# Performance work log

Hardware: AMD Instinct MI355X
Metric: run time of the kernel (lower is better)

Reference implementation:

```python
import jax, jax.numpy as jnp
import numpy as np

ALPHA = 0.2  # LeakyReLU slope
EPS = 1e-16


def _spgat_layer(x, W, a, row, col, N, concat):
    # h: [N, d]
    h = x @ W
    d = h.shape[1]
    # edge attention: a^T [h_row || h_col]  (pyGAT SpGAT: exp(-leakyrelu(.)))
    f_src = h @ a[:d]   # [N]
    f_dst = h @ a[d:]   # [N]
    e = jnp.exp(-jax.nn.leaky_relu(f_src[row] + f_dst[col], ALPHA))  # [E]
    denom = jax.ops.segment_sum(e, row, num_segments=N) + EPS        # [N]
    num = jax.ops.segment_sum(e[:, None] * h[col], row, num_segments=N)  # [N, d]
    out = num / denom[:, None]
    return jax.nn.elu(out) if concat else out


def _spgat(x, W1, a1, W2, a2, edges):
    row, col = edges[0], edges[1]
    N = x.shape[0]
    h = _spgat_layer(x, W1, a1, row, col, N, concat=True)
    h = _spgat_layer(h, W2, a2, row, col, N, concat=False)
    return jax.nn.elu(h)


def setup_inputs() -> dict:
    key = jax.random.key(0)
    ks = jax.random.split(key, 20)
    VOCAB, NFEAT = 50000, 300
    N_TW, L = 50000, 16
    UV = 50000
    E = 800000
    HID, JOINT, NCLASS = 64, 128, 2
    B = 4096

    inp = {}
    # integer structure (constants)
    inp['features_index'] = jax.random.randint(ks[0], (N_TW, L), 0, VOCAB, dtype=jnp.int32)
    inp['tw_edges'] = jax.random.randint(ks[1], (2, E), 0, N_TW, dtype=jnp.int32)
    inp['ut_edges'] = jax.random.randint(ks[2], (2, E), 0, UV, dtype=jnp.int32)
    inp['tw_graph_idx'] = jax.random.randint(ks[3], (B,), 0, N_TW, dtype=jnp.int32)
    inp['ut_graph_idx'] = jax.random.randint(ks[4], (B,), 0, UV, dtype=jnp.int32)
    # learned parameters
    inp['word_emb'] = jax.random.normal(ks[5], (VOCAB, NFEAT), jnp.float32) * 0.1
    inp['user_emb'] = jax.random.normal(ks[6], (UV, NFEAT), jnp.float32) * 0.1
    def gat_params(k, din, dh, dout):
        k1, k2, k3, k4 = jax.random.split(k, 4)
        return (jax.random.normal(k1, (din, dh), jnp.float32) * (1.0 / np.sqrt(din)),
                jax.random.normal(k2, (2 * dh,), jnp.float32) * 0.1,
                jax.random.normal(k3, (dh, dout), jnp.float32) * (1.0 / np.sqrt(dh)),
                jax.random.normal(k4, (2 * dout,), jnp.float32) * 0.1)
    inp['tw_W1'], inp['tw_a1'], inp['tw_W2'], inp['tw_a2'] = gat_params(ks[7], NFEAT, HID, JOINT)
    inp['tu_W1'], inp['tu_a1'], inp['tu_W2'], inp['tu_a2'] = gat_params(ks[8], NFEAT, HID, JOINT)
    inp['weight_W'] = jax.random.uniform(ks[9], (JOINT, JOINT), jnp.float32, -0.1, 0.1)
    inp['weight_proj'] = jax.random.uniform(ks[10], (JOINT, 1), jnp.float32, -0.1, 0.1)
    inp['out_W'] = jax.random.normal(ks[11], (NCLASS, JOINT), jnp.float32) * (1.0 / np.sqrt(JOINT))
    inp['out_b'] = jnp.zeros((NCLASS,), jnp.float32)
    return inp


def reference(word_emb, user_emb, tw_W1, tw_a1, tw_W2, tw_a2,
              tu_W1, tu_a1, tu_W2, tu_a2, weight_W, weight_proj,
              out_W, out_b, features_index, tw_edges, ut_edges,
              tw_graph_idx, ut_graph_idx):
    # tweet features: mean of word embeddings per tweet  [N_tw, nfeat]
    twt_X = word_emb[features_index].mean(axis=1)
    tw_X = _spgat(twt_X, tw_W1, tw_a1, tw_W2, tw_a2, tw_edges)   # [N_tw, joint]
    tu_X = _spgat(user_emb, tu_W1, tu_a1, tu_W2, tu_a2, ut_edges)  # [uV, joint]
    # attention-weighted fusion of the two views
    u_tw = jnp.tanh(tw_X @ weight_W)
    u_tu = jnp.tanh(tu_X @ weight_W)
    att_tw = jnp.mean(u_tw @ weight_proj, axis=0)  # [1]
    att_tu = jnp.mean(u_tu @ weight_proj, axis=0)  # [1]
    att = jax.nn.softmax(jnp.concatenate([att_tw, att_tu], axis=0))  # [2]
    feat = att[0] * tw_X[tw_graph_idx] + att[1] * tu_X[ut_graph_idx]  # [B, joint]
    logits = feat @ out_W.T + out_b
    return jax.nn.log_softmax(logits, axis=1)
```

## Files before the change

### kernel.cpp

```cpp
#include <hip/hip_runtime.h>
#include <hip/hip_bf16.h>

typedef __hip_bfloat16 bf16;
typedef unsigned int uint32;
typedef __attribute__((ext_vector_type(8))) short s8v;
typedef __attribute__((ext_vector_type(4))) short s4v;
typedef __attribute__((ext_vector_type(8))) short bf8v;
typedef __attribute__((ext_vector_type(4))) float f4v;

#define CAP 64
#define CAPSH 6

__device__ __forceinline__ float waveReduce(float v) {
#pragma unroll
    for (int o = 32; o > 0; o >>= 1) v += __shfl_xor(v, o, 64);
    return v;
}

__device__ __forceinline__ short f2bf(float x) {
    __hip_bfloat16 h = __float2bfloat16(x);
    return *reinterpret_cast<short*>(&h);
}
__device__ __forceinline__ float bf2f(short s) {
    return __uint_as_float(((uint32)(unsigned short)s) << 16);
}
__device__ __forceinline__ uint32 pack2(float x, float y) {
    return (uint32)(unsigned short)f2bf(x) | (((uint32)(unsigned short)f2bf(y)) << 16);
}
__device__ __forceinline__ float blo(uint32 d) { return __uint_as_float(d << 16); }
__device__ __forceinline__ float bhi(uint32 d) { return __uint_as_float(d & 0xffff0000u); }
__device__ __forceinline__ float felu(float x) { return x > 0.f ? x : __expf(x) - 1.f; }

struct WJobs {
    const float* src[5];
    short* dst[5];
    int K[5], N[5], KP[5], total[5];
    int* cursor;
    float* attsum;
    int N2;
};
__global__ void wtrans_all(WJobs jb) {
    int j = blockIdx.y;
    int i = blockIdx.x * blockDim.x + threadIdx.x;
    if (j == 5) {
        if (i < jb.N2) jb.cursor[i] = i << CAPSH;
        if (i < 2) jb.attsum[i] = 0.f;
        return;
    }
    if (i >= jb.total[j]) return;
    int KP = jb.KP[j];
    int n = i / KP, k = i - n * KP;
    jb.dst[j][i] = f2bf(k < jb.K[j] ? jb.src[j][(size_t)k * jb.N[j] + n] : 0.f);
}

struct GJob {
    const void* A;
    const short* Wt;
    const float* av;
    void* C;
    float* fs;
    float* fd;
    int M;
};
struct SJob {
    const int* rowA; const int* colA;
    const int* rowB; const int* colB;
    int* cursor; int* ecol;
    int E; int NTW; int nbg;
};

template <typename AT, int K, int KPAD, int N, int CSTORE, bool DO_F, bool DO_ATT, bool DO_SCAT>
__global__ __launch_bounds__(256) void mfma_gemm(GJob j0, GJob j1, int nb0,
                                                 float* __restrict__ attsum, int bnd, SJob sj) {
    constexpr int NT = N / 16;
    constexpr int NP = KPAD / 64;
    int t = threadIdx.x;

    if constexpr (DO_SCAT) {
        if ((int)blockIdx.x >= sj.nbg) {
            int i = ((int)blockIdx.x - sj.nbg) * 256 + t;
            if (i < sj.E) {
                int r = sj.rowA[i];
                int p0 = atomicAdd(&sj.cursor[r], 1);
                if (p0 < (r << CAPSH) + CAP) sj.ecol[p0] = sj.colA[i];
            } else if (i < 2 * sj.E) {
                int r = sj.NTW + sj.rowB[i - sj.E];
                int p0 = atomicAdd(&sj.cursor[r], 1);
                if (p0 < (r << CAPSH) + CAP) sj.ecol[p0] = sj.colB[i - sj.E];
            }
            return;
        }
    }

    __shared__ short As[64 * 72];
    __shared__ short Ws[N * 72];
    __shared__ float red[8];
    int lane = t & 63;
    int wid = t >> 6;
    int col = lane & 15;
    int quad = lane >> 4;

    int bid = blockIdx.x;
    bool sec = bid >= nb0;
    GJob J = sec ? j1 : j0;
    const AT* A = (const AT*)J.A;
    const short* Wt = J.Wt;
    const float* av = J.av;
    int M = J.M;
    int row0 = (sec ? bid - nb0 : bid) * 64;

    f4v acc[NT];
#pragma unroll
    for (int i = 0; i < NT; ++i) { f4v z = {0.f, 0.f, 0.f, 0.f}; acc[i] = z; }

    float4 ra[4];
    s8v rsa[2];
    s8v rb[NT / 2];

    auto issue = [&](int p) {
        int k0 = p * 64;
        if constexpr (sizeof(AT) == 4) {
            const float4* A4 = (const float4*)A;
            int f = t & 15, r0 = t >> 4;
#pragma unroll
            for (int r = 0; r < 4; ++r) {
                int gr = row0 + r0 + 16 * r;
                int f4i = (k0 >> 2) + f;
                float4 v = {0.f, 0.f, 0.f, 0.f};
                if (gr < M && f4i < K / 4) v = A4[(size_t)gr * (K / 4) + f4i];
                ra[r] = v;
            }
        } else {
            int c8 = t & 7, r0 = t >> 3;
#pragma unroll
            for (int r = 0; r < 2; ++r) {
                int gr = row0 + r0 + 32 * r;
                s8v v = {0, 0, 0, 0, 0, 0, 0, 0};
                if (gr < M) v = *(const s8v*)&A[(size_t)gr * K + k0 + c8 * 8];
                rsa[r] = v;
            }
        }
        {
            int c8 = t & 7, r0 = t >> 3;
#pragma unroll
            for (int r = 0; r < NT / 2; ++r)
                rb[r] = *(const s8v*)&Wt[(size_t)(r0 + 32 * r) * KPAD + k0 + c8 * 8];
        }
    };
    auto commit = [&]() {
        if constexpr (sizeof(AT) == 4) {
            int f = t & 15, r0 = t >> 4;
#pragma unroll
            for (int r = 0; r < 4; ++r) {
                float4 v = ra[r];
                s4v sv = {f2bf(v.x), f2bf(v.y), f2bf(v.z), f2bf(v.w)};
                *(s4v*)&As[(r0 + 16 * r) * 72 + f * 4] = sv;
            }
        } else {
            int c8 = t & 7, r0 = t >> 3;
#pragma unroll
            for (int r = 0; r < 2; ++r) *(s8v*)&As[(r0 + 32 * r) * 72 + c8 * 8] = rsa[r];
        }
        int c8 = t & 7, r0 = t >> 3;
#pragma unroll
        for (int r = 0; r < NT / 2; ++r) *(s8v*)&Ws[(r0 + 32 * r) * 72 + c8 * 8] = rb[r];
    };

    issue(0);
    for (int p = 0; p < NP; ++p) {
        __syncthreads();
        commit();
        __syncthreads();
        if (p + 1 < NP) issue(p + 1);
#pragma unroll
        for (int c2 = 0; c2 < 2; ++c2) {
            int ko = c2 * 32 + quad * 8;
            bf8v af = *(const bf8v*)&As[(wid * 16 + col) * 72 + ko];
#pragma unroll
            for (int nt = 0; nt < NT; ++nt) {
                bf8v bf = *(const bf8v*)&Ws[(nt * 16 + col) * 72 + ko];
                acc[nt] = __builtin_amdgcn_mfma_f32_16x16x32_bf16(af, bf, acc[nt], 0, 0, 0);
            }
        }
    }

    int mbase = row0 + wid * 16;
    if constexpr (CSTORE == 1) {
        float* C = (float*)J.C;
#pragma unroll
        for (int nt = 0; nt < NT; ++nt)
#pragma unroll
            for (int r = 0; r < 4; ++r) {
                int gr = mbase + quad * 4 + r;
                if (gr < M) C[(size_t)gr * N + nt * 16 + col] = acc[nt][r];
            }
    } else if constexpr (CSTORE == 2) {
        short* C = (short*)J.C;
#pragma unroll
        for (int nt = 0; nt < NT; ++nt)
#pragma unroll
            for (int r = 0; r < 4; ++r) {
                int gr = mbase + quad * 4 + r;
                if (gr < M) C[(size_t)gr * N + nt * 16 + col] = f2bf(acc[nt][r]);
            }
    }
    if constexpr (DO_F) {
        if (av) {
            float* fs = J.fs;
            float* fd = J.fd;
            float a0[NT], a1[NT];
#pragma unroll
            for (int nt = 0; nt < NT; ++nt) {
                a0[nt] = av[nt * 16 + col];
                a1[nt] = av[N + nt * 16 + col];
            }
#pragma unroll
            for (int r = 0; r < 4; ++r) {
                float p0 = 0.f, p1 = 0.f;
#pragma unroll
                for (int nt = 0; nt < NT; ++nt) {
                    p0 += acc[nt][r] * a0[nt];
                    p1 += acc[nt][r] * a1[nt];
                }
#pragma unroll
                for (int o = 8; o > 0; o >>= 1) {
                    p0 += __shfl_xor(p0, o, 64);
                    p1 += __shfl_xor(p1, o, 64);
                }
                int gr = mbase + quad * 4 + r;
                if (col == 0 && gr < M) { fs[gr] = p0; fd[gr] = p1; }
            }
        }
    }
    if constexpr (DO_ATT) {
        float s0 = 0.f, s1 = 0.f;
#pragma unroll
        for (int nt = 0; nt < NT; ++nt) {
            float pj = av[nt * 16 + col];
#pragma unroll
            for (int r = 0; r < 4; ++r) {
                int gr = mbase + quad * 4 + r;
                float v = tanhf(acc[nt][r]) * pj;
                if (gr < bnd) s0 += v; else s1 += v;
            }
        }
        s0 = waveReduce(s0);
        s1 = waveReduce(s1);
        if (lane == 0) { red[wid] = s0; red[4 + wid] = s1; }
        __syncthreads();
        if (t == 0) {
            atomicAdd(attsum + 0, red[0] + red[1] + red[2] + red[3]);
            atomicAdd(attsum + 1, red[4] + red[5] + red[6] + red[7]);
        }
    }
}

__global__ void gather_h64(const int* __restrict__ idx, const uint32* __restrict__ P,
                           const float* __restrict__ a,
                           short* __restrict__ H, float* __restrict__ fsv, float* __restrict__ fdv,
                           int N) {
    int wv = (blockIdx.x * blockDim.x + threadIdx.x) >> 6;
    int lane = threadIdx.x & 63;
    if (wv >= N) return;
    int hf = lane >> 5, li = lane & 31;
    const int* ip = idx + wv * 16;
    float a0 = 0.f, a1 = 0.f;
#pragma unroll
    for (int t = 0; t < 8; ++t) {
        int ind = ip[2 * t + hf];
        uint32 d = P[(size_t)ind * 32 + li];
        a0 += blo(d);
        a1 += bhi(d);
    }
    a0 += __shfl_xor(a0, 32, 64);
    a1 += __shfl_xor(a1, 32, 64);
    a0 *= 0.0625f;
    a1 *= 0.0625f;
    if (hf == 0) ((uint32*)H)[(size_t)wv * 32 + li] = pack2(a0, a1);
    float cp = hf ? 0.f : (a0 * a[2 * li] + a1 * a[2 * li + 1]);
    float cq = hf ? 0.f : (a0 * a[64 + 2 * li] + a1 * a[64 + 2 * li + 1]);
    float p = waveReduce(cp);
    float q = waveReduce(cq);
    if (lane == 0) { fsv[wv] = p; fdv[wv] = q; }
}

__global__ void agg64f_kernel(const int* __restrict__ cursor, const int* __restrict__ ecol,
                              const float* __restrict__ fs, const float* __restrict__ fd,
                              const uint32* __restrict__ hb, uint32* __restrict__ out,
                              int N2, int NTW) {
    int wv = (blockIdx.x * blockDim.x + threadIdx.x) >> 6;
    int lane = threadIdx.x & 63;
    if (wv >= N2) return;
    int s = wv << CAPSH;
    int ne = min(cursor[wv] - s, CAP);
    int coff = wv < NTW ? 0 : NTW;
    float fsr = fs[wv];
    int cl = 0;
    float el = 0.f;
    if (lane < ne) {
        cl = ecol[s + lane];
        float f = fsr + fd[coff + cl];
        el = __expf(-(f >= 0.f ? f : 0.2f * f));
    }
    int qd = lane >> 4, li = lane & 15;
    const uint2* h2 = (const uint2*)hb;
    float a0 = 0.f, a1 = 0.f, a2 = 0.f, a3 = 0.f, den = 0.f;
    for (int kb = 0; kb < ne; kb += 16) {
        int k0 = kb + qd, k1 = kb + 4 + qd, k2 = kb + 8 + qd, k3 = kb + 12 + qd;
        int c0 = __shfl(cl, k0, 64); float e0 = __shfl(el, k0, 64);
        int c1 = __shfl(cl, k1, 64); float e1 = __shfl(el, k1, 64);
        int c2 = __shfl(cl, k2, 64); float e2 = __shfl(el, k2, 64);
        int c3 = __shfl(cl, k3, 64); float e3 = __shfl(el, k3, 64);
        uint2 d0 = h2[(size_t)(coff + c0) * 16 + li];
        uint2 d1 = h2[(size_t)(coff + c1) * 16 + li];
        uint2 d2 = h2[(size_t)(coff + c2) * 16 + li];
        uint2 d3 = h2[(size_t)(coff + c3) * 16 + li];
        a0 += e0 * blo(d0.x) + e1 * blo(d1.x) + e2 * blo(d2.x) + e3 * blo(d3.x);
        a1 += e0 * bhi(d0.x) + e1 * bhi(d1.x) + e2 * bhi(d2.x) + e3 * bhi(d3.x);
        a2 += e0 * blo(d0.y) + e1 * blo(d1.y) + e2 * blo(d2.y) + e3 * blo(d3.y);
        a3 += e0 * bhi(d0.y) + e1 * bhi(d1.y) + e2 * bhi(d2.y) + e3 * bhi(d3.y);
        den += e0 + e1 + e2 + e3;
    }
    a0 += __shfl_xor(a0, 16, 64); a0 += __shfl_xor(a0, 32, 64);
    a1 += __shfl_xor(a1, 16, 64); a1 += __shfl_xor(a1, 32, 64);
    a2 += __shfl_xor(a2, 16, 64); a2 += __shfl_xor(a2, 32, 64);
    a3 += __shfl_xor(a3, 16, 64); a3 += __shfl_xor(a3, 32, 64);
    den += __shfl_xor(den, 16, 64); den += __shfl_xor(den, 32, 64);
    if (lane < 16) {
        float inv = 1.f / (den + 1e-16f);
        float v0 = felu(a0 * inv);
        float v1 = felu(a1 * inv);
        float v2 = felu(a2 * inv);
        float v3 = felu(a3 * inv);
        uint2 o = {pack2(v0, v1), pack2(v2, v3)};
        ((uint2*)out)[(size_t)wv * 16 + li] = o;
    }
}

__global__ void agg128f_kernel(const int* __restrict__ cursor, const int* __restrict__ ecol,
                               const float* __restrict__ fs, const float* __restrict__ fd,
                               const uint32* __restrict__ hb, uint32* __restrict__ out,
                               int N2, int NTW) {
    int wv = (blockIdx.x * blockDim.x + threadIdx.x) >> 6;
    int lane = threadIdx.x & 63;
    if (wv >= N2) return;
    int s = wv << CAPSH;
    int ne = min(cursor[wv] - s, CAP);
    int coff = wv < NTW ? 0 : NTW;
    float fsr = fs[wv];
    int cl = 0;
    float el = 0.f;
    if (lane < ne) {
        cl = ecol[s + lane];
        float f = fsr + fd[coff + cl];
        el = __expf(-(f >= 0.f ? f : 0.2f * f));
    }
    int hf = lane >> 5, li = lane & 31;
    const uint2* h2 = (const uint2*)hb;
    float a0 = 0.f, a1 = 0.f, a2 = 0.f, a3 = 0.f, den = 0.f;
    for (int kb = 0; kb < ne; kb += 8) {
        int k0 = kb + hf, k1 = kb + 2 + hf, k2 = kb + 4 + hf, k3 = kb + 6 + hf;
        int c0 = __shfl(cl, k0, 64); float e0 = __shfl(el, k0, 64);
        int c1 = __shfl(cl, k1, 64); float e1 = __shfl(el, k1, 64);
        int c2 = __shfl(cl, k2, 64); float e2 = __shfl(el, k2, 64);
        int c3 = __shfl(cl, k3, 64); float e3 = __shfl(el, k3, 64);
        uint2 d0 = h2[(size_t)(coff + c0) * 32 + li];
        uint2 d1 = h2[(size_t)(coff + c1) * 32 + li];
        uint2 d2 = h2[(size_t)(coff + c2) * 32 + li];
        uint2 d3 = h2[(size_t)(coff + c3) * 32 + li];
        a0 += e0 * blo(d0.x) + e1 * blo(d1.x) + e2 * blo(d2.x) + e3 * blo(d3.x);
        a1 += e0 * bhi(d0.x) + e1 * bhi(d1.x) + e2 * bhi(d2.x) + e3 * bhi(d3.x);
        a2 += e0 * blo(d0.y) + e1 * blo(d1.y) + e2 * blo(d2.y) + e3 * blo(d3.y);
        a3 += e0 * bhi(d0.y) + e1 * bhi(d1.y) + e2 * bhi(d2.y) + e3 * bhi(d3.y);
        den += e0 + e1 + e2 + e3;
    }
    a0 += __shfl_xor(a0, 32, 64);
    a1 += __shfl_xor(a1, 32, 64);
    a2 += __shfl_xor(a2, 32, 64);
    a3 += __shfl_xor(a3, 32, 64);
    den += __shfl_xor(den, 32, 64);
    if (hf == 0) {
        float inv = 1.f / (den + 1e-16f);
        float v0 = felu(a0 * inv);
        float v1 = felu(a1 * inv);
        float v2 = felu(a2 * inv);
        float v3 = felu(a3 * inv);
        uint2 o = {pack2(v0, v1), pack2(v2, v3)};
        ((uint2*)out)[(size_t)wv * 32 + li] = o;
    }
}

__global__ void final_kernel(const short* __restrict__ twX, const short* __restrict__ tuX,
                             const int* __restrict__ twi, const int* __restrict__ tui,
                             const float* __restrict__ attsum,
                             const float* __restrict__ outW, const float* __restrict__ outb,
                             float* __restrict__ out, int B, float invNtw, float invNuv) {
    int wave = (blockIdx.x * blockDim.x + threadIdx.x) >> 6;
    int lane = threadIdx.x & 63;
    if (wave >= B) return;
    float z0 = attsum[0] * invNtw, z1 = attsum[1] * invNuv;
    float m = fmaxf(z0, z1);
    float e0 = expf(z0 - m), e1 = expf(z1 - m);
    float a0 = e0 / (e0 + e1), a1 = e1 / (e0 + e1);
    int ti = twi[wave], ui = tui[wave];
    float l0 = 0.f, l1 = 0.f;
#pragma unroll
    for (int p = 0; p < 2; ++p) {
        int j = lane + 64 * p;
        float feat = a0 * bf2f(twX[(size_t)ti * 128 + j]) + a1 * bf2f(tuX[(size_t)ui * 128 + j]);
        l0 += feat * outW[j];
        l1 += feat * outW[128 + j];
    }
    l0 = waveReduce(l0);
    l1 = waveReduce(l1);
    if (lane == 0) {
        l0 += outb[0];
        l1 += outb[1];
        float mm = fmaxf(l0, l1);
        float lse = mm + logf(expf(l0 - mm) + expf(l1 - mm));
        out[wave * 2 + 0] = l0 - lse;
        out[wave * 2 + 1] = l1 - lse;
    }
}

extern "C" void kernel_launch(void* const* d_in, const int* in_sizes, int n_in,
                              void* d_out, int out_size, void* d_ws, size_t ws_size,
                              hipStream_t stream) {
    const int* features_index = (const int*)d_in[0];
    const int* tw_edges = (const int*)d_in[1];
    const int* ut_edges = (const int*)d_in[2];
    const int* tw_gidx = (const int*)d_in[3];
    const int* ut_gidx = (const int*)d_in[4];
    const float* word_emb = (const float*)d_in[5];
    const float* user_emb = (const float*)d_in[6];
    const float* tw_W1 = (const float*)d_in[7];
    const float* tw_a1 = (const float*)d_in[8];
    const float* tw_W2 = (const float*)d_in[9];
    const float* tw_a2 = (const float*)d_in[10];
    const float* tu_W1 = (const float*)d_in[11];
    const float* tu_a1 = (const float*)d_in[12];
    const float* tu_W2 = (const float*)d_in[13];
    const float* tu_a2 = (const float*)d_in[14];
    const float* weight_W = (const float*)d_in[15];
    const float* weight_proj = (const float*)d_in[16];
    const float* out_W = (const float*)d_in[17];
    const float* out_b = (const float*)d_in[18];

    const int E = in_sizes[1] / 2;
    const int NTW = in_sizes[0] / 16;
    const int VOCAB = in_sizes[5] / 300;
    const int UV = in_sizes[6] / 300;
    const int B = in_sizes[3];
    const int N2 = NTW + UV;

    char* ws = (char*)d_ws;
    size_t off = 0;
    auto carve = [&](size_t bytes) -> void* {
        void* p = ws + off;
        off += (bytes + 255) & ~(size_t)255;
        return p;
    };
    float* Pbuf = (float*)carve((size_t)VOCAB * 64 * sizeof(float));
    short* Hb1 = (short*)carve((size_t)N2 * 64 * sizeof(short));
    short* H2 = (short*)carve((size_t)N2 * 128 * sizeof(short));
    short* X = (short*)carve((size_t)N2 * 128 * sizeof(short));
    float* f_s = (float*)carve((size_t)N2 * sizeof(float));
    float* f_d = (float*)carve((size_t)N2 * sizeof(float));
    float* attsum = (float*)carve(256);
    int* cursor = (int*)carve((size_t)N2 * sizeof(int));
    int* ecol = (int*)carve((size_t)N2 * CAP * sizeof(int));
    short* Wt1tw = (short*)carve((size_t)64 * 320 * sizeof(short));
    short* Wt1tu = (short*)carve((size_t)64 * 320 * sizeof(short));
    short* Wt2tw = (short*)carve((size_t)128 * 64 * sizeof(short));
    short* Wt2tu = (short*)carve((size_t)128 * 64 * sizeof(short));
    short* Wta   = (short*)carve((size_t)128 * 128 * sizeof(short));
    short* num1 = ((size_t)VOCAB * 64 * sizeof(float) >= (size_t)N2 * 64 * sizeof(short))
                      ? (short*)Pbuf
                      : (short*)carve((size_t)N2 * 64 * sizeof(short));
    (void)ws_size; (void)n_in; (void)out_size;

    WJobs jb;
    jb.src[0] = tw_W1;    jb.dst[0] = Wt1tw; jb.K[0] = 300; jb.N[0] = 64;  jb.KP[0] = 320; jb.total[0] = 64 * 320;
    jb.src[1] = tu_W1;    jb.dst[1] = Wt1tu; jb.K[1] = 300; jb.N[1] = 64;  jb.KP[1] = 320; jb.total[1] = 64 * 320;
    jb.src[2] = tw_W2;    jb.dst[2] = Wt2tw; jb.K[2] = 64;  jb.N[2] = 128; jb.KP[2] = 64;  jb.total[2] = 128 * 64;
    jb.src[3] = tu_W2;    jb.dst[3] = Wt2tu; jb.K[3] = 64;  jb.N[3] = 128; jb.KP[3] = 64;  jb.total[3] = 128 * 64;
    jb.src[4] = weight_W; jb.dst[4] = Wta;   jb.K[4] = 128; jb.N[4] = 128; jb.KP[4] = 128; jb.total[4] = 128 * 128;
    jb.cursor = cursor;
    jb.attsum = attsum;
    jb.N2 = N2;
    {
        int gx = (64 * 320 + 255) / 256;
        int gc = (N2 + 255) / 256;
        if (gc > gx) gx = gc;
        dim3 g(gx, 6);
        wtrans_all<<<g, 256, 0, stream>>>(jb);
    }

    SJob sempty{nullptr, nullptr, nullptr, nullptr, nullptr, nullptr, 0, 0, 0};

    {
        GJob a{word_emb, Wt1tw, nullptr, Pbuf, nullptr, nullptr, VOCAB};
        GJob b{user_emb, Wt1tu, tu_a1, Hb1 + (size_t)NTW * 64, f_s + NTW, f_d + NTW, UV};
        int nbw = (VOCAB + 63) / 64, nbu = (UV + 63) / 64;
        int nbg = nbw + nbu;
        int nsc = (2 * E + 255) / 256;
        SJob sj{tw_edges, tw_edges + E, ut_edges, ut_edges + E, cursor, ecol, E, NTW, nbg};
        mfma_gemm<float, 300, 320, 64, 2, true, false, true><<<nbg + nsc, 256, 0, stream>>>(
            a, b, nbw, nullptr, 0, sj);
    }
    gather_h64<<<(NTW + 3) / 4, 256, 0, stream>>>(features_index, (const uint32*)Pbuf, tw_a1,
                                                  Hb1, f_s, f_d, NTW);

    agg64f_kernel<<<(N2 + 3) / 4, 256, 0, stream>>>(cursor, ecol, f_s, f_d,
                                                    (const uint32*)Hb1, (uint32*)num1, N2, NTW);

    {
        int nbtw = (NTW + 63) / 64, nbtu = (UV + 63) / 64;
        GJob a{num1, Wt2tw, tw_a2, H2, f_s, f_d, NTW};
        GJob b{num1 + (size_t)NTW * 64, Wt2tu, tu_a2, H2 + (size_t)NTW * 128,
               f_s + NTW, f_d + NTW, UV};
        mfma_gemm<short, 64, 64, 128, 2, true, false, false><<<nbtw + nbtu, 256, 0, stream>>>(
            a, b, nbtw, nullptr, 0, sempty);
    }

    agg128f_kernel<<<(N2 + 3) / 4, 256, 0, stream>>>(cursor, ecol, f_s, f_d,
                                                     (const uint32*)H2, (uint32*)X, N2, NTW);

    {
        GJob a{X, Wta, weight_proj, nullptr, nullptr, nullptr, N2};
        int nb = (N2 + 63) / 64;
        mfma_gemm<short, 128, 128, 128, 0, false, true, false><<<nb, 256, 0, stream>>>(
            a, a, nb, attsum, NTW, sempty);
    }

    final_kernel<<<(B + 3) / 4, 256, 0, stream>>>(X, X + (size_t)NTW * 128, tw_gidx, ut_gidx,
                                                  attsum, out_W, out_b, (float*)d_out, B,
                                                  1.0f / (float)NTW, 1.0f / (float)UV);
}
```

Baseline: 486.3 us.

## Two-pass edge bucketing: stage edges by row window before CSR scatter

The direct scatter of edges into per-row slots with random global atomics is replaced by two passes. First, the GEMM-side scatter blocks bucket packed (row, col) edges into 128 staging bins keyed by row window and block slot, using wave-aggregated atomics. Then extra blocks in the gather kernel replay each bin and do the per-row cursor atomics within a localized row range, aiming for better cache locality. This adds an extra pass over the edges and a staging buffer that aliases X. It also relies on column ids fitting in 16 bits and bins not overflowing SCAP, otherwise edges are silently dropped.

```diff
diff --git a/kernel.cpp b/kernel.cpp
--- a/kernel.cpp
+++ b/kernel.cpp
@@ -10,6 +10,7 @@
 
 #define CAP 64
 #define CAPSH 6
+#define WSH 14
 
 __device__ __forceinline__ float waveReduce(float v) {
 #pragma unroll
@@ -37,6 +38,7 @@
     int K[5], N[5], KP[5], total[5];
     int* cursor;
     float* attsum;
+    int* gcount;
     int N2;
 };
 __global__ void wtrans_all(WJobs jb) {
@@ -45,6 +47,7 @@
     if (j == 5) {
         if (i < jb.N2) jb.cursor[i] = i << CAPSH;
         if (i < 2) jb.attsum[i] = 0.f;
+        if (i < 128) jb.gcount[i] = 0;
         return;
     }
     if (i >= jb.total[j]) return;
@@ -65,8 +68,8 @@
 struct SJob {
     const int* rowA; const int* colA;
     const int* rowB; const int* colB;
-    int* cursor; int* ecol;
-    int E; int NTW; int nbg;
+    uint32* stage; int* gcount;
+    int E; int NTW; int nbg; int SCAP;
 };
 
 template <typename AT, int K, int KPAD, int N, int CSTORE, bool DO_F, bool DO_ATT, bool DO_SCAT>
@@ -78,15 +81,33 @@
 
     if constexpr (DO_SCAT) {
         if ((int)blockIdx.x >= sj.nbg) {
-            int i = ((int)blockIdx.x - sj.nbg) * 256 + t;
+            int bb = (int)blockIdx.x - sj.nbg;
+            int i = bb * 256 + t;
+            int lane = t & 63;
+            int slot = bb & 15;
+            int r = -1, c = 0;
             if (i < sj.E) {
-                int r = sj.rowA[i];
-                int p0 = atomicAdd(&sj.cursor[r], 1);
-                if (p0 < (r << CAPSH) + CAP) sj.ecol[p0] = sj.colA[i];
+                r = sj.rowA[i]; c = sj.colA[i];
             } else if (i < 2 * sj.E) {
-                int r = sj.NTW + sj.rowB[i - sj.E];
-                int p0 = atomicAdd(&sj.cursor[r], 1);
-                if (p0 < (r << CAPSH) + CAP) sj.ecol[p0] = sj.colB[i - sj.E];
+                r = sj.NTW + sj.rowB[i - sj.E]; c = sj.colB[i - sj.E];
+            }
+            int w = r >> WSH;
+            uint32 val = ((uint32)(r & ((1 << WSH) - 1)) << 16) | (uint32)c;
+#pragma unroll
+            for (int k = 0; k < 8; ++k) {
+                unsigned long long m = __ballot(r >= 0 && w == k);
+                if (m == 0ull) continue;
+                int cnt = __popcll(m);
+                int lead = __ffsll((long long)m) - 1;
+                int base = 0;
+                if (lane == lead) base = atomicAdd(&sj.gcount[k * 16 + slot], cnt);
+                base = __shfl(base, lead, 64);
+                if (r >= 0 && w == k) {
+                    int myoff = __popcll(m & ((1ull << lane) - 1ull));
+                    int pos = base + myoff;
+                    if (pos < sj.SCAP)
+                        sj.stage[((size_t)(k * 16 + slot)) * sj.SCAP + pos] = val;
+                }
             }
             return;
         }
@@ -258,16 +279,37 @@
 __global__ void gather_h64(const int* __restrict__ idx, const uint32* __restrict__ P,
                            const float* __restrict__ a,
                            short* __restrict__ H, float* __restrict__ fsv, float* __restrict__ fdv,
-                           int N) {
-    int wv = (blockIdx.x * blockDim.x + threadIdx.x) >> 6;
-    int lane = threadIdx.x & 63;
+                           int N,
+                           const uint32* __restrict__ stage, const int* __restrict__ gcount,
+                           int SCAP, int* __restrict__ cursor, int* __restrict__ ecol, int nPB) {
+    int t = threadIdx.x;
+    if ((int)blockIdx.x < nPB) {
+        int b = blockIdx.x;
+        int w = b & 7;
+        int rest = b >> 3;
+        int slot = rest & 15;
+        int chunk = rest >> 4;
+        int cnt = min(gcount[w * 16 + slot], SCAP);
+        int jend = min(chunk * 4096 + 4096, cnt);
+        const uint32* sp = stage + ((size_t)(w * 16 + slot)) * SCAP;
+        for (int j = chunk * 4096 + t; j < jend; j += 256) {
+            uint32 v = sp[j];
+            int r = (w << WSH) + (int)(v >> 16);
+            int c = (int)(v & 0xffffu);
+            int p = atomicAdd(&cursor[r], 1);
+            if (p < (r << CAPSH) + CAP) ecol[p] = c;
+        }
+        return;
+    }
+    int wv = (((int)blockIdx.x - nPB) * 256 + t) >> 6;
+    int lane = t & 63;
     if (wv >= N) return;
     int hf = lane >> 5, li = lane & 31;
     const int* ip = idx + wv * 16;
     float a0 = 0.f, a1 = 0.f;
 #pragma unroll
-    for (int t = 0; t < 8; ++t) {
-        int ind = ip[2 * t + hf];
+    for (int u = 0; u < 8; ++u) {
+        int ind = ip[2 * u + hf];
         uint32 d = P[(size_t)ind * 32 + li];
         a0 += blo(d);
         a1 += bhi(d);
@@ -469,6 +511,7 @@
     float* attsum = (float*)carve(256);
     int* cursor = (int*)carve((size_t)N2 * sizeof(int));
     int* ecol = (int*)carve((size_t)N2 * CAP * sizeof(int));
+    int* gcount = (int*)carve(128 * sizeof(int));
     short* Wt1tw = (short*)carve((size_t)64 * 320 * sizeof(short));
     short* Wt1tu = (short*)carve((size_t)64 * 320 * sizeof(short));
     short* Wt2tw = (short*)carve((size_t)128 * 64 * sizeof(short));
@@ -477,6 +520,11 @@
     short* num1 = ((size_t)VOCAB * 64 * sizeof(float) >= (size_t)N2 * 64 * sizeof(short))
                       ? (short*)Pbuf
                       : (short*)carve((size_t)N2 * 64 * sizeof(short));
+    int perSlot = (2 * E) / 128;
+    int SCAP = ((perSlot * 13 / 8) + 4095) / 4096 * 4096;
+    int chunks = SCAP / 4096;
+    int nPB = 128 * chunks;
+    uint32* stage = (uint32*)X;
     (void)ws_size; (void)n_in; (void)out_size;
 
     WJobs jb;
@@ -487,6 +535,7 @@
     jb.src[4] = weight_W; jb.dst[4] = Wta;   jb.K[4] = 128; jb.N[4] = 128; jb.KP[4] = 128; jb.total[4] = 128 * 128;
     jb.cursor = cursor;
     jb.attsum = attsum;
+    jb.gcount = gcount;
     jb.N2 = N2;
     {
         int gx = (64 * 320 + 255) / 256;
@@ -496,7 +545,7 @@
         wtrans_all<<<g, 256, 0, stream>>>(jb);
     }
 
-    SJob sempty{nullptr, nullptr, nullptr, nullptr, nullptr, nullptr, 0, 0, 0};
+    SJob sempty{nullptr, nullptr, nullptr, nullptr, nullptr, nullptr, 0, 0, 0, 0};
 
     {
         GJob a{word_emb, Wt1tw, nullptr, Pbuf, nullptr, nullptr, VOCAB};
@@ -504,12 +553,14 @@
         int nbw = (VOCAB + 63) / 64, nbu = (UV + 63) / 64;
         int nbg = nbw + nbu;
         int nsc = (2 * E + 255) / 256;
-        SJob sj{tw_edges, tw_edges + E, ut_edges, ut_edges + E, cursor, ecol, E, NTW, nbg};
+        SJob sj{tw_edges, tw_edges + E, ut_edges, ut_edges + E, stage, gcount, E, NTW, nbg, SCAP};
         mfma_gemm<float, 300, 320, 64, 2, true, false, true><<<nbg + nsc, 256, 0, stream>>>(
             a, b, nbw, nullptr, 0, sj);
     }
-    gather_h64<<<(NTW + 3) / 4, 256, 0, stream>>>(features_index, (const uint32*)Pbuf, tw_a1,
-                                                  Hb1, f_s, f_d, NTW);
+
+    gather_h64<<<nPB + (NTW + 3) / 4, 256, 0, stream>>>(features_index, (const uint32*)Pbuf,
+                                                        tw_a1, Hb1, f_s, f_d, NTW,
+                                                        stage, gcount, SCAP, cursor, ecol, nPB);
 
     agg64f_kernel<<<(N2 + 3) / 4, 256, 0, stream>>>(cursor, ecol, f_s, f_d,
                                                     (const uint32*)Hb1, (uint32*)num1, N2, NTW);
```

New measurement: 792.5 us. +63.0%, slower.

## Partition edge-scatter atomics by row window aligned to XCD block mapping

Applied to the files above, without the earlier changes.

The edge-bucketing scatter fused into the first GEMM launch now runs with eight times as many blocks. Each block takes a row window from `blockIdx & 7` and only performs the `atomicAdd` and `ecol` write for edges whose destination row falls in that window. The aim is to keep the atomics on a given range of cursor counters within one XCD's L2, given round-robin block placement across the eight XCDs, instead of spreading contended atomics across the chip. In exchange every edge index is read eight times and many more scatter blocks are launched. A loop variable in the gather kernel is also renamed.

```diff
diff --git a/kernel.cpp b/kernel.cpp
--- a/kernel.cpp
+++ b/kernel.cpp
@@ -66,7 +66,7 @@
     const int* rowA; const int* colA;
     const int* rowB; const int* colB;
     int* cursor; int* ecol;
-    int E; int NTW; int nbg;
+    int E; int NTW; int nbg; int Wsize;
 };
 
 template <typename AT, int K, int KPAD, int N, int CSTORE, bool DO_F, bool DO_ATT, bool DO_SCAT>
@@ -78,15 +78,20 @@
 
     if constexpr (DO_SCAT) {
         if ((int)blockIdx.x >= sj.nbg) {
-            int i = ((int)blockIdx.x - sj.nbg) * 256 + t;
+            int bb = (int)blockIdx.x - sj.nbg;
+            int w = (int)blockIdx.x & 7;
+            int i = (bb >> 3) * 256 + t;
+            int lo = w * sj.Wsize;
+            int hi = lo + sj.Wsize;
+            int r = -1, c = 0;
             if (i < sj.E) {
-                int r = sj.rowA[i];
+                r = sj.rowA[i]; c = sj.colA[i];
+            } else if (i < 2 * sj.E) {
+                r = sj.NTW + sj.rowB[i - sj.E]; c = sj.colB[i - sj.E];
+            }
+            if (r >= lo && r < hi) {
                 int p0 = atomicAdd(&sj.cursor[r], 1);
-                if (p0 < (r << CAPSH) + CAP) sj.ecol[p0] = sj.colA[i];
-            } else if (i < 2 * sj.E) {
-                int r = sj.NTW + sj.rowB[i - sj.E];
-                int p0 = atomicAdd(&sj.cursor[r], 1);
-                if (p0 < (r << CAPSH) + CAP) sj.ecol[p0] = sj.colB[i - sj.E];
+                if (p0 < (r << CAPSH) + CAP) sj.ecol[p0] = c;
             }
             return;
         }
@@ -266,8 +271,8 @@
     const int* ip = idx + wv * 16;
     float a0 = 0.f, a1 = 0.f;
 #pragma unroll
-    for (int t = 0; t < 8; ++t) {
-        int ind = ip[2 * t + hf];
+    for (int u = 0; u < 8; ++u) {
+        int ind = ip[2 * u + hf];
         uint32 d = P[(size_t)ind * 32 + li];
         a0 += blo(d);
         a1 += bhi(d);
@@ -496,15 +501,16 @@
         wtrans_all<<<g, 256, 0, stream>>>(jb);
     }
 
-    SJob sempty{nullptr, nullptr, nullptr, nullptr, nullptr, nullptr, 0, 0, 0};
+    SJob sempty{nullptr, nullptr, nullptr, nullptr, nullptr, nullptr, 0, 0, 0, 0};
 
     {
         GJob a{word_emb, Wt1tw, nullptr, Pbuf, nullptr, nullptr, VOCAB};
         GJob b{user_emb, Wt1tu, tu_a1, Hb1 + (size_t)NTW * 64, f_s + NTW, f_d + NTW, UV};
         int nbw = (VOCAB + 63) / 64, nbu = (UV + 63) / 64;
         int nbg = nbw + nbu;
-        int nsc = (2 * E + 255) / 256;
-        SJob sj{tw_edges, tw_edges + E, ut_edges, ut_edges + E, cursor, ecol, E, NTW, nbg};
+        int nsc = 8 * ((2 * E + 255) / 256);
+        int Wsize = (N2 + 7) / 8;
+        SJob sj{tw_edges, tw_edges + E, ut_edges, ut_edges + E, cursor, ecol, E, NTW, nbg, Wsize};
         mfma_gemm<float, 300, 320, 64, 2, true, false, true><<<nbg + nsc, 256, 0, stream>>>(
             a, b, nbw, nullptr, 0, sj);
     }
```

New measurement: 435.8 us. -10.4%, faster.
